# Optimization experiments

Hardware: AMD Instinct MI355X
Metric: run time of the kernel (lower is better)

Reference implementation:

```python
import jax, jax.numpy as jnp
import numpy as np

V, E, H, S, T, B = 32000, 200, 512, 64, 64, 64

def _u(key, shape, k):
    return jax.random.uniform(key, shape, jnp.float32, -k, k)

def setup_inputs() -> dict:
    key = jax.random.key(0)
    ks = jax.random.split(key, 25)
    kH = float(1.0 / np.sqrt(H))
    inp = {}
    inp['src'] = jax.random.randint(ks[0], (S, B), 0, V)
    inp['target'] = jax.random.randint(ks[1], (T, B), 0, V)
    inp['tf_mask'] = jax.random.randint(ks[2], (T,), 0, 2)
    inp['enc_embed'] = _u(ks[3], (V, E), 0.1)
    inp['dec_embed'] = _u(ks[4], (V, E), 0.1)
    i = 5
    for pre in ('e', 'd'):
        for l, din in ((0, E), (1, H)):
            inp[f'{pre}W_ih{l}'] = _u(ks[i], (4 * H, din), kH); i += 1
            inp[f'{pre}W_hh{l}'] = _u(ks[i], (4 * H, H), kH); i += 1
            inp[f'{pre}b_ih{l}'] = _u(ks[i], (4 * H,), kH); i += 1
            inp[f'{pre}b_hh{l}'] = _u(ks[i], (4 * H,), kH); i += 1
    inp['fc_W'] = _u(ks[i], (V, H), kH)
    inp['fc_b'] = _u(ks[i + 1], (V,), kH)
    return inp

def _lstm_cell(h, c, x, Wih, Whh, bih, bhh):
    # PyTorch gate order: input, forget, cell(g), output
    gates = x @ Wih.T + h @ Whh.T + (bih + bhh)
    i, f, g, o = jnp.split(gates, 4, axis=-1)
    c = jax.nn.sigmoid(f) * c + jax.nn.sigmoid(i) * jnp.tanh(g)
    h = jax.nn.sigmoid(o) * jnp.tanh(c)
    return h, c

def reference(enc_embed, eW_ih0, eW_hh0, eb_ih0, eb_hh0, eW_ih1, eW_hh1, eb_ih1, eb_hh1,
              dec_embed, dW_ih0, dW_hh0, db_ih0, db_hh0, dW_ih1, dW_hh1, db_ih1, db_hh1,
              fc_W, fc_b, src, target, tf_mask):
    batch = src.shape[1]
    z = jnp.zeros((batch, H), jnp.float32)

    # ---- Encoder: 2-layer LSTM over src, keep final (hidden, cell) ----
    emb = enc_embed[src]  # [S, B, E]
    def enc_step(carry, x_t):
        h0, c0, h1, c1 = carry
        h0, c0 = _lstm_cell(h0, c0, x_t, eW_ih0, eW_hh0, eb_ih0, eb_hh0)
        h1, c1 = _lstm_cell(h1, c1, h0, eW_ih1, eW_hh1, eb_ih1, eb_hh1)
        return (h0, c0, h1, c1), None
    (h0, c0, h1, c1), _ = jax.lax.scan(enc_step, (z, z, z, z), emb)

    def dec_step(carry, inp):
        h0, c0, h1, c1, x = carry
        t_tok, tf = inp
        e = dec_embed[x]  # [B, E]
        h0, c0 = _lstm_cell(h0, c0, e, dW_ih0, dW_hh0, db_ih0, db_hh0)
        h1, c1 = _lstm_cell(h1, c1, h0, dW_ih1, dW_hh1, db_ih1, db_hh1)
        logits = h1 @ fc_W.T + fc_b  # [B, V]
        pred = jnp.argmax(logits, axis=1).astype(x.dtype)
        nxt = jnp.where(tf > 0, t_tok, pred)
        return (h0, c0, h1, c1, nxt), logits

    x0 = target[0]
    _, logits_seq = jax.lax.scan(dec_step, (h0, c0, h1, c1, x0),
                                 (target[1:], tf_mask[1:]))
    vocab = fc_b.shape[0]
    outputs = jnp.concatenate(
        [jnp.zeros((1, batch, vocab), jnp.float32), logits_seq], axis=0)
    return outputs
```

## Files before the change

### kernel.cpp

```cpp
#include <hip/hip_runtime.h>
#include <math.h>

#define VSIZE 32000
#define EDIM  200
#define HDIM  512
#define SLEN  64
#define TLEN  64
#define BATCH 64

__device__ __forceinline__ float dot4(const float4 a, const float4 b) {
    return a.x * b.x + a.y * b.y + a.z * b.z + a.w * b.w;
}

__device__ __forceinline__ float sigmoidf_(float x) { return 1.0f / (1.0f + expf(-x)); }

__global__ void init_zero(float* __restrict__ out0, float* __restrict__ wsf) {
    const size_t n_out = (size_t)BATCH * VSIZE;
    const size_t n_ws  = 6u * 32768u;
    size_t i = (size_t)blockIdx.x * blockDim.x + threadIdx.x;
    size_t stride = (size_t)gridDim.x * blockDim.x;
    for (size_t k = i; k < n_out + n_ws; k += stride) {
        if (k < n_out) out0[k] = 0.0f;
        else           wsf[k - n_out] = 0.0f;
    }
}

__global__ __launch_bounds__(256) void lstm_cell_l0(
    const float* __restrict__ embed, const int* __restrict__ toks,
    const float* __restrict__ Wih, const float* __restrict__ Whh,
    const float* __restrict__ bih, const float* __restrict__ bhh,
    const float* __restrict__ hT_in, float* __restrict__ hT_out,
    float* __restrict__ cT)
{
    __shared__ float xs[(EDIM / 4) * BATCH * 4];

    const int tid = threadIdx.x;
    {
        const int bb = tid >> 2, q = tid & 3;
        const int tok = toks[bb];
        const float4* src4 = (const float4*)(embed + (size_t)tok * EDIM);
        for (int j = q; j < EDIM / 4; j += 4) {
            float4 v = src4[j];
            float* dst = &xs[j * 256 + bb * 4];
            dst[0] = v.x; dst[1] = v.y; dst[2] = v.z; dst[3] = v.w;
        }
    }
    __syncthreads();

    const int b  = tid & 63;
    const int hl = tid >> 6;
    const int h  = blockIdx.x * 4 + hl;

    float acc0 = 0.f, acc1 = 0.f, acc2 = 0.f, acc3 = 0.f;

    {
        const float4* w0 = (const float4*)(Wih + (size_t)(h        ) * EDIM);
        const float4* w1 = (const float4*)(Wih + (size_t)(h +  512 ) * EDIM);
        const float4* w2 = (const float4*)(Wih + (size_t)(h + 1024 ) * EDIM);
        const float4* w3 = (const float4*)(Wih + (size_t)(h + 1536 ) * EDIM);
        for (int j = 0; j < EDIM / 4; ++j) {
            float4 xv = *(const float4*)&xs[j * 256 + b * 4];
            acc0 += dot4(xv, w0[j]);
            acc1 += dot4(xv, w1[j]);
            acc2 += dot4(xv, w2[j]);
            acc3 += dot4(xv, w3[j]);
        }
    }
    {
        const float4* u0 = (const float4*)(Whh + (size_t)(h        ) * HDIM);
        const float4* u1 = (const float4*)(Whh + (size_t)(h +  512 ) * HDIM);
        const float4* u2 = (const float4*)(Whh + (size_t)(h + 1024 ) * HDIM);
        const float4* u3 = (const float4*)(Whh + (size_t)(h + 1536 ) * HDIM);
        const float4* hin = (const float4*)hT_in;
        for (int j = 0; j < HDIM / 4; ++j) {
            float4 xv = hin[j * 64 + b];
            acc0 += dot4(xv, u0[j]);
            acc1 += dot4(xv, u1[j]);
            acc2 += dot4(xv, u2[j]);
            acc3 += dot4(xv, u3[j]);
        }
    }

    acc0 += bih[h]        + bhh[h];
    acc1 += bih[h +  512] + bhh[h +  512];
    acc2 += bih[h + 1024] + bhh[h + 1024];
    acc3 += bih[h + 1536] + bhh[h + 1536];

    const int cidx = (h >> 2) * 256 + b * 4 + (h & 3);
    float c_old = cT[cidx];
    float gi = sigmoidf_(acc0);
    float gf = sigmoidf_(acc1);
    float gg = tanhf(acc2);
    float go = sigmoidf_(acc3);
    float c_new = gf * c_old + gi * gg;
    float h_new = go * tanhf(c_new);
    cT[cidx]     = c_new;
    hT_out[cidx] = h_new;
}

__global__ __launch_bounds__(256) void lstm_cell_l1(
    const float* __restrict__ xT,
    const float* __restrict__ Wih, const float* __restrict__ Whh,
    const float* __restrict__ bih, const float* __restrict__ bhh,
    const float* __restrict__ hT_in, float* __restrict__ hT_out,
    float* __restrict__ cT)
{
    const int tid = threadIdx.x;
    const int b  = tid & 63;
    const int hl = tid >> 6;
    const int h  = blockIdx.x * 4 + hl;

    float acc0 = 0.f, acc1 = 0.f, acc2 = 0.f, acc3 = 0.f;

    {
        const float4* w0 = (const float4*)(Wih + (size_t)(h        ) * HDIM);
        const float4* w1 = (const float4*)(Wih + (size_t)(h +  512 ) * HDIM);
        const float4* w2 = (const float4*)(Wih + (size_t)(h + 1024 ) * HDIM);
        const float4* w3 = (const float4*)(Wih + (size_t)(h + 1536 ) * HDIM);
        const float4* xin = (const float4*)xT;
        for (int j = 0; j < HDIM / 4; ++j) {
            float4 xv = xin[j * 64 + b];
            acc0 += dot4(xv, w0[j]);
            acc1 += dot4(xv, w1[j]);
            acc2 += dot4(xv, w2[j]);
            acc3 += dot4(xv, w3[j]);
        }
    }
    {
        const float4* u0 = (const float4*)(Whh + (size_t)(h        ) * HDIM);
        const float4* u1 = (const float4*)(Whh + (size_t)(h +  512 ) * HDIM);
        const float4* u2 = (const float4*)(Whh + (size_t)(h + 1024 ) * HDIM);
        const float4* u3 = (const float4*)(Whh + (size_t)(h + 1536 ) * HDIM);
        const float4* hin = (const float4*)hT_in;
        for (int j = 0; j < HDIM / 4; ++j) {
            float4 xv = hin[j * 64 + b];
            acc0 += dot4(xv, u0[j]);
            acc1 += dot4(xv, u1[j]);
            acc2 += dot4(xv, u2[j]);
            acc3 += dot4(xv, u3[j]);
        }
    }

    acc0 += bih[h]        + bhh[h];
    acc1 += bih[h +  512] + bhh[h +  512];
    acc2 += bih[h + 1024] + bhh[h + 1024];
    acc3 += bih[h + 1536] + bhh[h + 1536];

    const int cidx = (h >> 2) * 256 + b * 4 + (h & 3);
    float c_old = cT[cidx];
    float gi = sigmoidf_(acc0);
    float gf = sigmoidf_(acc1);
    float gg = tanhf(acc2);
    float go = sigmoidf_(acc3);
    float c_new = gf * c_old + gi * gg;
    float h_new = go * tanhf(c_new);
    cT[cidx]     = c_new;
    hT_out[cidx] = h_new;
}

__global__ __launch_bounds__(256) void fc_kernel(
    const float* __restrict__ h1T, const float* __restrict__ fcW,
    const float* __restrict__ fcb, float* __restrict__ out_slice)
{
    const int tid = threadIdx.x;
    const int b  = tid & 63;
    const int vl = tid >> 6;
    const int v  = blockIdx.x * 4 + vl;

    const float4* w  = (const float4*)(fcW + (size_t)v * HDIM);
    const float4* hv = (const float4*)h1T;
    float acc = fcb[v];
    for (int j = 0; j < HDIM / 4; ++j) {
        acc += dot4(hv[j * 64 + b], w[j]);
    }
    out_slice[(size_t)b * VSIZE + v] = acc;
}

__global__ __launch_bounds__(256) void argmax_tok(
    const float* __restrict__ logits, const int* __restrict__ target_row,
    const int* __restrict__ tf_p, int* __restrict__ tok)
{
    const int b = blockIdx.x;
    const float* row = logits + (size_t)b * VSIZE;
    float best = -INFINITY;
    int bidx = 0;
    for (int v = threadIdx.x; v < VSIZE; v += 256) {
        float val = row[v];
        if (val > best) { best = val; bidx = v; }
    }
    __shared__ float sv[256];
    __shared__ int   si[256];
    sv[threadIdx.x] = best; si[threadIdx.x] = bidx;
    __syncthreads();
    for (int s = 128; s > 0; s >>= 1) {
        if (threadIdx.x < s) {
            float ov = sv[threadIdx.x + s]; int oi = si[threadIdx.x + s];
            float mv = sv[threadIdx.x];     int mi = si[threadIdx.x];
            if (ov > mv || (ov == mv && oi < mi)) { sv[threadIdx.x] = ov; si[threadIdx.x] = oi; }
        }
        __syncthreads();
    }
    if (threadIdx.x == 0) {
        tok[b] = (*tf_p > 0) ? target_row[b] : si[0];
    }
}

extern "C" void kernel_launch(void* const* d_in, const int* in_sizes, int n_in,
                              void* d_out, int out_size, void* d_ws, size_t ws_size,
                              hipStream_t stream)
{
    const int*   src      = (const int*)  d_in[0];
    const int*   target   = (const int*)  d_in[1];
    const int*   tf_mask  = (const int*)  d_in[2];
    const float* enc_emb  = (const float*)d_in[3];
    const float* dec_emb  = (const float*)d_in[4];
    const float* eW_ih0 = (const float*)d_in[5],  *eW_hh0 = (const float*)d_in[6];
    const float* eb_ih0 = (const float*)d_in[7],  *eb_hh0 = (const float*)d_in[8];
    const float* eW_ih1 = (const float*)d_in[9],  *eW_hh1 = (const float*)d_in[10];
    const float* eb_ih1 = (const float*)d_in[11], *eb_hh1 = (const float*)d_in[12];
    const float* dW_ih0 = (const float*)d_in[13], *dW_hh0 = (const float*)d_in[14];
    const float* db_ih0 = (const float*)d_in[15], *db_hh0 = (const float*)d_in[16];
    const float* dW_ih1 = (const float*)d_in[17], *dW_hh1 = (const float*)d_in[18];
    const float* db_ih1 = (const float*)d_in[19], *db_hh1 = (const float*)d_in[20];
    const float* fcW    = (const float*)d_in[21];
    const float* fcb    = (const float*)d_in[22];

    float* out = (float*)d_out;
    float* ws  = (float*)d_ws;

    float* h0a = ws;
    float* h0b = ws + 32768;
    float* h1a = ws + 2 * 32768;
    float* h1b = ws + 3 * 32768;
    float* c0  = ws + 4 * 32768;
    float* c1  = ws + 5 * 32768;
    int*   tok = (int*)(ws + 6 * 32768);

    init_zero<<<1024, 256, 0, stream>>>(out, ws);

    float* h0in = h0a; float* h0out = h0b;
    float* h1in = h1a; float* h1out = h1b;
    for (int t = 0; t < SLEN; ++t) {
        lstm_cell_l0<<<128, 256, 0, stream>>>(enc_emb, src + t * BATCH,
                                              eW_ih0, eW_hh0, eb_ih0, eb_hh0,
                                              h0in, h0out, c0);
        lstm_cell_l1<<<128, 256, 0, stream>>>(h0out,
                                              eW_ih1, eW_hh1, eb_ih1, eb_hh1,
                                              h1in, h1out, c1);
        float* tmp;
        tmp = h0in; h0in = h0out; h0out = tmp;
        tmp = h1in; h1in = h1out; h1out = tmp;
    }

    const int* toks = target;
    for (int j = 0; j < TLEN - 1; ++j) {
        lstm_cell_l0<<<128, 256, 0, stream>>>(dec_emb, toks,
                                              dW_ih0, dW_hh0, db_ih0, db_hh0,
                                              h0in, h0out, c0);
        lstm_cell_l1<<<128, 256, 0, stream>>>(h0out,
                                              dW_ih1, dW_hh1, db_ih1, db_hh1,
                                              h1in, h1out, c1);
        float* slice = out + (size_t)(j + 1) * BATCH * VSIZE;
        fc_kernel<<<VSIZE / 4, 256, 0, stream>>>(h1out, fcW, fcb, slice);
        if (j < TLEN - 2) {
            argmax_tok<<<BATCH, 256, 0, stream>>>(slice, target + (j + 1) * BATCH,
                                                  tf_mask + (j + 1), tok);
        }
        toks = tok;
        float* tmp;
        tmp = h0in; h0in = h0out; h0out = tmp;
        tmp = h1in; h1in = h1out; h1out = tmp;
    }
}
```

Before: 29.65 ms.

## Fuse whole seq2seq into one persistent cooperative kernel with grid barriers

Replaces about 320 separate kernel launches with a single persistent cooperative kernel of 256 blocks that sync through a custom atomic grid barrier. Cell state is kept in shared memory, and the recurrent matmul is split across waves along the K dimension. The FC layer computes 125 vocab rows per block with a per-block argmax candidate, which removes the full re-read of the logits for argmax. The cost is barrier latency and reliance on all blocks being co-resident; if the cooperative launch fails, the fallback normal launch could deadlock.

```diff
diff --git a/kernel.cpp b/kernel.cpp
--- a/kernel.cpp
+++ b/kernel.cpp
@@ -7,268 +7,366 @@
 #define SLEN  64
 #define TLEN  64
 #define BATCH 64
+#define NBLK  256
+#define NTHR  512
+#define VPB   125
+
+struct Params {
+  const int   *src, *target, *tf_mask;
+  const float *enc_emb, *dec_emb;
+  const float *eW_ih0, *eW_hh0, *eb_ih0, *eb_hh0;
+  const float *eW_ih1, *eW_hh1, *eb_ih1, *eb_hh1;
+  const float *dW_ih0, *dW_hh0, *db_ih0, *db_hh0;
+  const float *dW_ih1, *dW_hh1, *db_ih1, *db_hh1;
+  const float *fcW, *fcb;
+  float *out;
+  float *h0a, *h0b, *h1a, *h1b;
+  float *cand_val;
+  int   *cand_idx;
+  int   *tok;
+  unsigned *bar;
+};
 
 __device__ __forceinline__ float dot4(const float4 a, const float4 b) {
-    return a.x * b.x + a.y * b.y + a.z * b.z + a.w * b.w;
-}
-
+  return a.x * b.x + a.y * b.y + a.z * b.z + a.w * b.w;
+}
 __device__ __forceinline__ float sigmoidf_(float x) { return 1.0f / (1.0f + expf(-x)); }
 
-__global__ void init_zero(float* __restrict__ out0, float* __restrict__ wsf) {
-    const size_t n_out = (size_t)BATCH * VSIZE;
-    const size_t n_ws  = 6u * 32768u;
-    size_t i = (size_t)blockIdx.x * blockDim.x + threadIdx.x;
-    size_t stride = (size_t)gridDim.x * blockDim.x;
-    for (size_t k = i; k < n_out + n_ws; k += stride) {
-        if (k < n_out) out0[k] = 0.0f;
-        else           wsf[k - n_out] = 0.0f;
-    }
-}
-
-__global__ __launch_bounds__(256) void lstm_cell_l0(
-    const float* __restrict__ embed, const int* __restrict__ toks,
+__device__ __forceinline__ void gsync(unsigned* bar) {
+  __syncthreads();
+  if (threadIdx.x == 0) {
+    __threadfence();
+    unsigned gen = __hip_atomic_load(&bar[1], __ATOMIC_RELAXED, __HIP_MEMORY_SCOPE_AGENT);
+    unsigned n = __hip_atomic_fetch_add(&bar[0], 1u, __ATOMIC_ACQ_REL, __HIP_MEMORY_SCOPE_AGENT);
+    if (n == NBLK - 1u) {
+      __hip_atomic_store(&bar[0], 0u, __ATOMIC_RELAXED, __HIP_MEMORY_SCOPE_AGENT);
+      __hip_atomic_store(&bar[1], gen + 1u, __ATOMIC_RELEASE, __HIP_MEMORY_SCOPE_AGENT);
+    } else {
+      while (__hip_atomic_load(&bar[1], __ATOMIC_ACQUIRE, __HIP_MEMORY_SCOPE_AGENT) == gen)
+        __builtin_amdgcn_s_sleep(1);
+    }
+    __threadfence();
+  }
+  __syncthreads();
+}
+
+__device__ __forceinline__ void lstm_l0(
+    const float* __restrict__ emb, const int* __restrict__ toks,
     const float* __restrict__ Wih, const float* __restrict__ Whh,
     const float* __restrict__ bih, const float* __restrict__ bhh,
-    const float* __restrict__ hT_in, float* __restrict__ hT_out,
-    float* __restrict__ cT)
-{
-    __shared__ float xs[(EDIM / 4) * BATCH * 4];
-
-    const int tid = threadIdx.x;
-    {
-        const int bb = tid >> 2, q = tid & 3;
-        const int tok = toks[bb];
-        const float4* src4 = (const float4*)(embed + (size_t)tok * EDIM);
-        for (int j = q; j < EDIM / 4; j += 4) {
-            float4 v = src4[j];
-            float* dst = &xs[j * 256 + bb * 4];
-            dst[0] = v.x; dst[1] = v.y; dst[2] = v.z; dst[3] = v.w;
-        }
-    }
-    __syncthreads();
-
-    const int b  = tid & 63;
-    const int hl = tid >> 6;
-    const int h  = blockIdx.x * 4 + hl;
-
-    float acc0 = 0.f, acc1 = 0.f, acc2 = 0.f, acc3 = 0.f;
-
-    {
-        const float4* w0 = (const float4*)(Wih + (size_t)(h        ) * EDIM);
-        const float4* w1 = (const float4*)(Wih + (size_t)(h +  512 ) * EDIM);
-        const float4* w2 = (const float4*)(Wih + (size_t)(h + 1024 ) * EDIM);
-        const float4* w3 = (const float4*)(Wih + (size_t)(h + 1536 ) * EDIM);
-        for (int j = 0; j < EDIM / 4; ++j) {
-            float4 xv = *(const float4*)&xs[j * 256 + b * 4];
-            acc0 += dot4(xv, w0[j]);
-            acc1 += dot4(xv, w1[j]);
-            acc2 += dot4(xv, w2[j]);
-            acc3 += dot4(xv, w3[j]);
-        }
-    }
-    {
-        const float4* u0 = (const float4*)(Whh + (size_t)(h        ) * HDIM);
-        const float4* u1 = (const float4*)(Whh + (size_t)(h +  512 ) * HDIM);
-        const float4* u2 = (const float4*)(Whh + (size_t)(h + 1024 ) * HDIM);
-        const float4* u3 = (const float4*)(Whh + (size_t)(h + 1536 ) * HDIM);
-        const float4* hin = (const float4*)hT_in;
-        for (int j = 0; j < HDIM / 4; ++j) {
-            float4 xv = hin[j * 64 + b];
-            acc0 += dot4(xv, u0[j]);
-            acc1 += dot4(xv, u1[j]);
-            acc2 += dot4(xv, u2[j]);
-            acc3 += dot4(xv, u3[j]);
-        }
-    }
-
-    acc0 += bih[h]        + bhh[h];
-    acc1 += bih[h +  512] + bhh[h +  512];
-    acc2 += bih[h + 1024] + bhh[h + 1024];
-    acc3 += bih[h + 1536] + bhh[h + 1536];
-
-    const int cidx = (h >> 2) * 256 + b * 4 + (h & 3);
-    float c_old = cT[cidx];
-    float gi = sigmoidf_(acc0);
-    float gf = sigmoidf_(acc1);
-    float gg = tanhf(acc2);
-    float go = sigmoidf_(acc3);
-    float c_new = gf * c_old + gi * gg;
-    float h_new = go * tanhf(c_new);
-    cT[cidx]     = c_new;
-    hT_out[cidx] = h_new;
-}
-
-__global__ __launch_bounds__(256) void lstm_cell_l1(
+    const float* __restrict__ h_in, float* __restrict__ h_out,
+    float* cls, float* part, bool skip_h)
+{
+  const int tid = threadIdx.x;
+  const int b = tid & 63, wv = tid >> 6;
+  const int hl = wv & 1, kc = wv >> 1;
+  const int h = blockIdx.x * 2 + hl;
+
+  float a0 = 0.f, a1 = 0.f, a2 = 0.f, a3 = 0.f;
+  if (kc == 0) {
+    const int tokid = toks[b];
+    const float4* xr = (const float4*)(emb + (size_t)tokid * EDIM);
+    const float4* w0 = (const float4*)(Wih + (size_t)(h       ) * EDIM);
+    const float4* w1 = (const float4*)(Wih + (size_t)(h +  512) * EDIM);
+    const float4* w2 = (const float4*)(Wih + (size_t)(h + 1024) * EDIM);
+    const float4* w3 = (const float4*)(Wih + (size_t)(h + 1536) * EDIM);
+#pragma unroll 10
+    for (int j = 0; j < EDIM / 4; ++j) {
+      float4 x = xr[j];
+      a0 += dot4(x, w0[j]); a1 += dot4(x, w1[j]);
+      a2 += dot4(x, w2[j]); a3 += dot4(x, w3[j]);
+    }
+  } else if (!skip_h) {
+    const int j0 = (kc == 1) ? 0 : (kc == 2) ? 43 : 86;
+    const int j1 = (kc == 1) ? 43 : (kc == 2) ? 86 : 128;
+    const float4* hr = (const float4*)h_in;
+    const float4* u0 = (const float4*)(Whh + (size_t)(h       ) * HDIM);
+    const float4* u1 = (const float4*)(Whh + (size_t)(h +  512) * HDIM);
+    const float4* u2 = (const float4*)(Whh + (size_t)(h + 1024) * HDIM);
+    const float4* u3 = (const float4*)(Whh + (size_t)(h + 1536) * HDIM);
+    for (int j = j0; j < j1; ++j) {
+      float4 x = hr[j * 64 + b];
+      a0 += dot4(x, u0[j]); a1 += dot4(x, u1[j]);
+      a2 += dot4(x, u2[j]); a3 += dot4(x, u3[j]);
+    }
+  }
+  part[wv * 256 +       b] = a0;
+  part[wv * 256 +  64 + b] = a1;
+  part[wv * 256 + 128 + b] = a2;
+  part[wv * 256 + 192 + b] = a3;
+  __syncthreads();
+  if (tid < 128) {
+    const int bb = tid & 63, hl2 = tid >> 6;
+    const int h2 = blockIdx.x * 2 + hl2;
+    float g0 = 0.f, g1 = 0.f, g2 = 0.f, g3 = 0.f;
+#pragma unroll
+    for (int k = 0; k < 4; ++k) {
+      const float* pp = part + (k * 2 + hl2) * 256;
+      g0 += pp[bb]; g1 += pp[64 + bb]; g2 += pp[128 + bb]; g3 += pp[192 + bb];
+    }
+    g0 += bih[h2]        + bhh[h2];
+    g1 += bih[h2 +  512] + bhh[h2 +  512];
+    g2 += bih[h2 + 1024] + bhh[h2 + 1024];
+    g3 += bih[h2 + 1536] + bhh[h2 + 1536];
+    float c_old = cls[hl2 * 64 + bb];
+    float gi = sigmoidf_(g0), gf = sigmoidf_(g1);
+    float gg = tanhf(g2),     go = sigmoidf_(g3);
+    float cn = gf * c_old + gi * gg;
+    float hn = go * tanhf(cn);
+    cls[hl2 * 64 + bb] = cn;
+    h_out[(h2 >> 2) * 256 + bb * 4 + (h2 & 3)] = hn;
+  }
+}
+
+__device__ __forceinline__ void lstm_l1(
     const float* __restrict__ xT,
     const float* __restrict__ Wih, const float* __restrict__ Whh,
     const float* __restrict__ bih, const float* __restrict__ bhh,
-    const float* __restrict__ hT_in, float* __restrict__ hT_out,
-    float* __restrict__ cT)
-{
-    const int tid = threadIdx.x;
-    const int b  = tid & 63;
-    const int hl = tid >> 6;
-    const int h  = blockIdx.x * 4 + hl;
-
-    float acc0 = 0.f, acc1 = 0.f, acc2 = 0.f, acc3 = 0.f;
-
-    {
-        const float4* w0 = (const float4*)(Wih + (size_t)(h        ) * HDIM);
-        const float4* w1 = (const float4*)(Wih + (size_t)(h +  512 ) * HDIM);
-        const float4* w2 = (const float4*)(Wih + (size_t)(h + 1024 ) * HDIM);
-        const float4* w3 = (const float4*)(Wih + (size_t)(h + 1536 ) * HDIM);
-        const float4* xin = (const float4*)xT;
-        for (int j = 0; j < HDIM / 4; ++j) {
-            float4 xv = xin[j * 64 + b];
-            acc0 += dot4(xv, w0[j]);
-            acc1 += dot4(xv, w1[j]);
-            acc2 += dot4(xv, w2[j]);
-            acc3 += dot4(xv, w3[j]);
-        }
-    }
-    {
-        const float4* u0 = (const float4*)(Whh + (size_t)(h        ) * HDIM);
-        const float4* u1 = (const float4*)(Whh + (size_t)(h +  512 ) * HDIM);
-        const float4* u2 = (const float4*)(Whh + (size_t)(h + 1024 ) * HDIM);
-        const float4* u3 = (const float4*)(Whh + (size_t)(h + 1536 ) * HDIM);
-        const float4* hin = (const float4*)hT_in;
-        for (int j = 0; j < HDIM / 4; ++j) {
-            float4 xv = hin[j * 64 + b];
-            acc0 += dot4(xv, u0[j]);
-            acc1 += dot4(xv, u1[j]);
-            acc2 += dot4(xv, u2[j]);
-            acc3 += dot4(xv, u3[j]);
-        }
-    }
-
-    acc0 += bih[h]        + bhh[h];
-    acc1 += bih[h +  512] + bhh[h +  512];
-    acc2 += bih[h + 1024] + bhh[h + 1024];
-    acc3 += bih[h + 1536] + bhh[h + 1536];
-
-    const int cidx = (h >> 2) * 256 + b * 4 + (h & 3);
-    float c_old = cT[cidx];
-    float gi = sigmoidf_(acc0);
-    float gf = sigmoidf_(acc1);
-    float gg = tanhf(acc2);
-    float go = sigmoidf_(acc3);
-    float c_new = gf * c_old + gi * gg;
-    float h_new = go * tanhf(c_new);
-    cT[cidx]     = c_new;
-    hT_out[cidx] = h_new;
-}
-
-__global__ __launch_bounds__(256) void fc_kernel(
+    const float* __restrict__ h_in, float* __restrict__ h_out,
+    float* cls, float* part, bool skip_h)
+{
+  const int tid = threadIdx.x;
+  const int b = tid & 63, wv = tid >> 6;
+  const int hl = wv & 1, kc = wv >> 1;
+  const int h = blockIdx.x * 2 + hl;
+
+  float a0 = 0.f, a1 = 0.f, a2 = 0.f, a3 = 0.f;
+  if (kc < 2) {
+    const int j0 = kc * 64;
+    const float4* xr = (const float4*)xT;
+    const float4* w0 = (const float4*)(Wih + (size_t)(h       ) * HDIM);
+    const float4* w1 = (const float4*)(Wih + (size_t)(h +  512) * HDIM);
+    const float4* w2 = (const float4*)(Wih + (size_t)(h + 1024) * HDIM);
+    const float4* w3 = (const float4*)(Wih + (size_t)(h + 1536) * HDIM);
+    for (int j = j0; j < j0 + 64; ++j) {
+      float4 x = xr[j * 64 + b];
+      a0 += dot4(x, w0[j]); a1 += dot4(x, w1[j]);
+      a2 += dot4(x, w2[j]); a3 += dot4(x, w3[j]);
+    }
+  } else if (!skip_h) {
+    const int j0 = (kc - 2) * 64;
+    const float4* hr = (const float4*)h_in;
+    const float4* u0 = (const float4*)(Whh + (size_t)(h       ) * HDIM);
+    const float4* u1 = (const float4*)(Whh + (size_t)(h +  512) * HDIM);
+    const float4* u2 = (const float4*)(Whh + (size_t)(h + 1024) * HDIM);
+    const float4* u3 = (const float4*)(Whh + (size_t)(h + 1536) * HDIM);
+    for (int j = j0; j < j0 + 64; ++j) {
+      float4 x = hr[j * 64 + b];
+      a0 += dot4(x, u0[j]); a1 += dot4(x, u1[j]);
+      a2 += dot4(x, u2[j]); a3 += dot4(x, u3[j]);
+    }
+  }
+  part[wv * 256 +       b] = a0;
+  part[wv * 256 +  64 + b] = a1;
+  part[wv * 256 + 128 + b] = a2;
+  part[wv * 256 + 192 + b] = a3;
+  __syncthreads();
+  if (tid < 128) {
+    const int bb = tid & 63, hl2 = tid >> 6;
+    const int h2 = blockIdx.x * 2 + hl2;
+    float g0 = 0.f, g1 = 0.f, g2 = 0.f, g3 = 0.f;
+#pragma unroll
+    for (int k = 0; k < 4; ++k) {
+      const float* pp = part + (k * 2 + hl2) * 256;
+      g0 += pp[bb]; g1 += pp[64 + bb]; g2 += pp[128 + bb]; g3 += pp[192 + bb];
+    }
+    g0 += bih[h2]        + bhh[h2];
+    g1 += bih[h2 +  512] + bhh[h2 +  512];
+    g2 += bih[h2 + 1024] + bhh[h2 + 1024];
+    g3 += bih[h2 + 1536] + bhh[h2 + 1536];
+    float c_old = cls[hl2 * 64 + bb];
+    float gi = sigmoidf_(g0), gf = sigmoidf_(g1);
+    float gg = tanhf(g2),     go = sigmoidf_(g3);
+    float cn = gf * c_old + gi * gg;
+    float hn = go * tanhf(cn);
+    cls[hl2 * 64 + bb] = cn;
+    h_out[(h2 >> 2) * 256 + bb * 4 + (h2 & 3)] = hn;
+  }
+}
+
+__device__ __forceinline__ void fc_phase(
     const float* __restrict__ h1T, const float* __restrict__ fcW,
-    const float* __restrict__ fcb, float* __restrict__ out_slice)
-{
-    const int tid = threadIdx.x;
-    const int b  = tid & 63;
-    const int vl = tid >> 6;
-    const int v  = blockIdx.x * 4 + vl;
-
-    const float4* w  = (const float4*)(fcW + (size_t)v * HDIM);
-    const float4* hv = (const float4*)h1T;
-    float acc = fcb[v];
-    for (int j = 0; j < HDIM / 4; ++j) {
-        acc += dot4(hv[j * 64 + b], w[j]);
-    }
-    out_slice[(size_t)b * VSIZE + v] = acc;
-}
-
-__global__ __launch_bounds__(256) void argmax_tok(
-    const float* __restrict__ logits, const int* __restrict__ target_row,
-    const int* __restrict__ tf_p, int* __restrict__ tok)
-{
-    const int b = blockIdx.x;
-    const float* row = logits + (size_t)b * VSIZE;
-    float best = -INFINITY;
-    int bidx = 0;
-    for (int v = threadIdx.x; v < VSIZE; v += 256) {
-        float val = row[v];
-        if (val > best) { best = val; bidx = v; }
-    }
-    __shared__ float sv[256];
-    __shared__ int   si[256];
-    sv[threadIdx.x] = best; si[threadIdx.x] = bidx;
+    const float* __restrict__ fcb, float* __restrict__ out_slice,
+    float* ltile, float* amv, int* ami,
+    float* __restrict__ cand_val, int* __restrict__ cand_idx)
+{
+  const int tid = threadIdx.x;
+  const int b = tid & 63, vl = tid >> 6;
+  const int vstart = blockIdx.x * VPB;
+  const float4* __restrict__ hr = (const float4*)h1T;
+
+  const float4* wp[16];
+  float acc[16];
+#pragma unroll
+  for (int j = 0; j < 16; ++j) {
+    int vloc = j * 8 + vl;
+    if (vloc > VPB - 1) vloc = VPB - 1;
+    wp[j] = (const float4*)(fcW + (size_t)(vstart + vloc) * HDIM);
+    acc[j] = 0.f;
+  }
+  for (int kb = 0; kb < HDIM / 4; ++kb) {
+    float4 hv = hr[kb * 64 + b];
+#pragma unroll
+    for (int j = 0; j < 16; ++j) acc[j] += dot4(hv, wp[j][kb]);
+  }
+
+  float best = -INFINITY; int bidx = 0x7fffffff;
+#pragma unroll
+  for (int j = 0; j < 16; ++j) {
+    const int vloc = j * 8 + vl;
+    if (vloc < VPB) {
+      const int v = vstart + vloc;
+      const float val = acc[j] + fcb[v];
+      ltile[vloc * 65 + b] = val;
+      if (val > best) { best = val; bidx = v; }
+    }
+  }
+  amv[vl * 64 + b] = best;
+  ami[vl * 64 + b] = bidx;
+  __syncthreads();
+
+  if (tid < 64) {
+    float bv = amv[tid]; int bi = ami[tid];
+#pragma unroll
+    for (int k = 1; k < 8; ++k) {
+      float ov = amv[k * 64 + tid]; int oi = ami[k * 64 + tid];
+      if (ov > bv || (ov == bv && oi < bi)) { bv = ov; bi = oi; }
+    }
+    cand_val[tid * NBLK + blockIdx.x] = bv;
+    cand_idx[tid * NBLK + blockIdx.x] = bi;
+  }
+
+  {
+    const int vloc = tid & 127, bq = tid >> 7;
+    if (vloc < VPB) {
+#pragma unroll
+      for (int bo = 0; bo < 16; ++bo) {
+        const int bb = bo * 4 + bq;
+        out_slice[(size_t)bb * VSIZE + vstart + vloc] = ltile[vloc * 65 + bb];
+      }
+    }
+  }
+}
+
+__device__ __forceinline__ void amax_phase(
+    const float* __restrict__ cand_val, const int* __restrict__ cand_idx,
+    const int* __restrict__ target_row, const int* __restrict__ tfp,
+    int* __restrict__ tok, float* sv, int* si)
+{
+  if (blockIdx.x >= 64) return;
+  const int b = blockIdx.x, tid = threadIdx.x;
+  if (tid < 256) { sv[tid] = cand_val[b * NBLK + tid]; si[tid] = cand_idx[b * NBLK + tid]; }
+  __syncthreads();
+  for (int s = 128; s > 0; s >>= 1) {
+    if (tid < s) {
+      float ov = sv[tid + s]; int oi = si[tid + s];
+      if (ov > sv[tid] || (ov == sv[tid] && oi < si[tid])) { sv[tid] = ov; si[tid] = oi; }
+    }
     __syncthreads();
-    for (int s = 128; s > 0; s >>= 1) {
-        if (threadIdx.x < s) {
-            float ov = sv[threadIdx.x + s]; int oi = si[threadIdx.x + s];
-            float mv = sv[threadIdx.x];     int mi = si[threadIdx.x];
-            if (ov > mv || (ov == mv && oi < mi)) { sv[threadIdx.x] = ov; si[threadIdx.x] = oi; }
-        }
-        __syncthreads();
-    }
-    if (threadIdx.x == 0) {
-        tok[b] = (*tf_p > 0) ? target_row[b] : si[0];
-    }
+  }
+  if (tid == 0) tok[b] = (*tfp > 0) ? target_row[b] : si[0];
+}
+
+__global__ void bar_init(unsigned* __restrict__ bar) {
+  if (threadIdx.x < 2) bar[threadIdx.x] = 0u;
+}
+
+__global__ __launch_bounds__(NTHR, 2) void seq2seq_kernel(Params p)
+{
+  __shared__ float part[8 * 256];
+  __shared__ float ltile[VPB * 65];
+  __shared__ float amv[512];
+  __shared__ int   ami[512];
+  __shared__ float sv[256];
+  __shared__ int   si[256];
+  __shared__ float c0ls[128], c1ls[128];
+
+  const int tid = threadIdx.x;
+  if (tid < 128) { c0ls[tid] = 0.f; c1ls[tid] = 0.f; }
+
+  {
+    float4* o4 = (float4*)p.out;
+    const int total = BATCH * VSIZE / 4;
+    for (int i = blockIdx.x * NTHR + tid; i < total; i += NBLK * NTHR)
+      o4[i] = make_float4(0.f, 0.f, 0.f, 0.f);
+  }
+  __syncthreads();
+
+  float* h0bufs[2] = { p.h0a, p.h0b };
+  float* h1bufs[2] = { p.h1a, p.h1b };
+
+  for (int t = 0; t < SLEN; ++t) {
+    const float* h0in = h0bufs[t & 1];  float* h0out = h0bufs[(t & 1) ^ 1];
+    const float* h1in = h1bufs[t & 1];  float* h1out = h1bufs[(t & 1) ^ 1];
+    lstm_l0(p.enc_emb, p.src + t * BATCH, p.eW_ih0, p.eW_hh0, p.eb_ih0, p.eb_hh0,
+            h0in, h0out, c0ls, part, t == 0);
+    gsync(p.bar);
+    lstm_l1(h0out, p.eW_ih1, p.eW_hh1, p.eb_ih1, p.eb_hh1,
+            h1in, h1out, c1ls, part, t == 0);
+    gsync(p.bar);
+  }
+
+  if (blockIdx.x == 0 && tid < 64) p.tok[tid] = p.target[tid];
+  gsync(p.bar);
+
+  for (int j = 0; j < TLEN - 1; ++j) {
+    const float* h0in = h0bufs[j & 1];  float* h0out = h0bufs[(j & 1) ^ 1];
+    const float* h1in = h1bufs[j & 1];  float* h1out = h1bufs[(j & 1) ^ 1];
+    lstm_l0(p.dec_emb, p.tok, p.dW_ih0, p.dW_hh0, p.db_ih0, p.db_hh0,
+            h0in, h0out, c0ls, part, false);
+    gsync(p.bar);
+    lstm_l1(h0out, p.dW_ih1, p.dW_hh1, p.db_ih1, p.db_hh1,
+            h1in, h1out, c1ls, part, false);
+    gsync(p.bar);
+    fc_phase(h1out, p.fcW, p.fcb, p.out + (size_t)(j + 1) * BATCH * VSIZE,
+             ltile, amv, ami, p.cand_val, p.cand_idx);
+    if (j < TLEN - 2) {
+      gsync(p.bar);
+      amax_phase(p.cand_val, p.cand_idx, p.target + (j + 1) * BATCH,
+                 p.tf_mask + (j + 1), p.tok, sv, si);
+      gsync(p.bar);
+    }
+  }
 }
 
 extern "C" void kernel_launch(void* const* d_in, const int* in_sizes, int n_in,
                               void* d_out, int out_size, void* d_ws, size_t ws_size,
                               hipStream_t stream)
 {
-    const int*   src      = (const int*)  d_in[0];
-    const int*   target   = (const int*)  d_in[1];
-    const int*   tf_mask  = (const int*)  d_in[2];
-    const float* enc_emb  = (const float*)d_in[3];
-    const float* dec_emb  = (const float*)d_in[4];
-    const float* eW_ih0 = (const float*)d_in[5],  *eW_hh0 = (const float*)d_in[6];
-    const float* eb_ih0 = (const float*)d_in[7],  *eb_hh0 = (const float*)d_in[8];
-    const float* eW_ih1 = (const float*)d_in[9],  *eW_hh1 = (const float*)d_in[10];
-    const float* eb_ih1 = (const float*)d_in[11], *eb_hh1 = (const float*)d_in[12];
-    const float* dW_ih0 = (const float*)d_in[13], *dW_hh0 = (const float*)d_in[14];
-    const float* db_ih0 = (const float*)d_in[15], *db_hh0 = (const float*)d_in[16];
-    const float* dW_ih1 = (const float*)d_in[17], *dW_hh1 = (const float*)d_in[18];
-    const float* db_ih1 = (const float*)d_in[19], *db_hh1 = (const float*)d_in[20];
-    const float* fcW    = (const float*)d_in[21];
-    const float* fcb    = (const float*)d_in[22];
-
-    float* out = (float*)d_out;
-    float* ws  = (float*)d_ws;
-
-    float* h0a = ws;
-    float* h0b = ws + 32768;
-    float* h1a = ws + 2 * 32768;
-    float* h1b = ws + 3 * 32768;
-    float* c0  = ws + 4 * 32768;
-    float* c1  = ws + 5 * 32768;
-    int*   tok = (int*)(ws + 6 * 32768);
-
-    init_zero<<<1024, 256, 0, stream>>>(out, ws);
-
-    float* h0in = h0a; float* h0out = h0b;
-    float* h1in = h1a; float* h1out = h1b;
-    for (int t = 0; t < SLEN; ++t) {
-        lstm_cell_l0<<<128, 256, 0, stream>>>(enc_emb, src + t * BATCH,
-                                              eW_ih0, eW_hh0, eb_ih0, eb_hh0,
-                                              h0in, h0out, c0);
-        lstm_cell_l1<<<128, 256, 0, stream>>>(h0out,
-                                              eW_ih1, eW_hh1, eb_ih1, eb_hh1,
-                                              h1in, h1out, c1);
-        float* tmp;
-        tmp = h0in; h0in = h0out; h0out = tmp;
-        tmp = h1in; h1in = h1out; h1out = tmp;
-    }
-
-    const int* toks = target;
-    for (int j = 0; j < TLEN - 1; ++j) {
-        lstm_cell_l0<<<128, 256, 0, stream>>>(dec_emb, toks,
-                                              dW_ih0, dW_hh0, db_ih0, db_hh0,
-                                              h0in, h0out, c0);
-        lstm_cell_l1<<<128, 256, 0, stream>>>(h0out,
-                                              dW_ih1, dW_hh1, db_ih1, db_hh1,
-                                              h1in, h1out, c1);
-        float* slice = out + (size_t)(j + 1) * BATCH * VSIZE;
-        fc_kernel<<<VSIZE / 4, 256, 0, stream>>>(h1out, fcW, fcb, slice);
-        if (j < TLEN - 2) {
-            argmax_tok<<<BATCH, 256, 0, stream>>>(slice, target + (j + 1) * BATCH,
-                                                  tf_mask + (j + 1), tok);
-        }
-        toks = tok;
-        float* tmp;
-        tmp = h0in; h0in = h0out; h0out = tmp;
-        tmp = h1in; h1in = h1out; h1out = tmp;
-    }
-}
+  Params p;
+  p.src     = (const int*)  d_in[0];
+  p.target  = (const int*)  d_in[1];
+  p.tf_mask = (const int*)  d_in[2];
+  p.enc_emb = (const float*)d_in[3];
+  p.dec_emb = (const float*)d_in[4];
+  p.eW_ih0 = (const float*)d_in[5];  p.eW_hh0 = (const float*)d_in[6];
+  p.eb_ih0 = (const float*)d_in[7];  p.eb_hh0 = (const float*)d_in[8];
+  p.eW_ih1 = (const float*)d_in[9];  p.eW_hh1 = (const float*)d_in[10];
+  p.eb_ih1 = (const float*)d_in[11]; p.eb_hh1 = (const float*)d_in[12];
+  p.dW_ih0 = (const float*)d_in[13]; p.dW_hh0 = (const float*)d_in[14];
+  p.db_ih0 = (const float*)d_in[15]; p.db_hh0 = (const float*)d_in[16];
+  p.dW_ih1 = (const float*)d_in[17]; p.dW_hh1 = (const float*)d_in[18];
+  p.db_ih1 = (const float*)d_in[19]; p.db_hh1 = (const float*)d_in[20];
+  p.fcW    = (const float*)d_in[21];
+  p.fcb    = (const float*)d_in[22];
+  p.out = (float*)d_out;
+
+  float* ws = (float*)d_ws;
+  p.h0a = ws;
+  p.h0b = ws + 32768;
+  p.h1a = ws + 2 * 32768;
+  p.h1b = ws + 3 * 32768;
+  p.cand_val = ws + 4 * 32768;
+  p.cand_idx = (int*)(ws + 4 * 32768 + 16384);
+  p.tok      = (int*)(ws + 4 * 32768 + 32768);
+  p.bar      = (unsigned*)(ws + 4 * 32768 + 32768 + 64);
+
+  bar_init<<<1, 64, 0, stream>>>(p.bar);
+
+  void* args[] = { (void*)&p };
+  hipError_t err = hipLaunchCooperativeKernel((void*)seq2seq_kernel,
+                                              dim3(NBLK), dim3(NTHR), args, 0, stream);
+  if (err != hipSuccess) {
+    hipLaunchKernelGGL(seq2seq_kernel, dim3(NBLK), dim3(NTHR), 0, stream, p);
+  }
+}
```

New measurement: 31.19 ms. 5.2% more time.
